# Performance work log

Hardware: AMD Instinct MI355X
Metric: run time of the kernel (lower is better)

The kernel has to match this reference:

```python
import jax, jax.numpy as jnp
import numpy as np

QSIGN = jnp.array([1.0, -1.0, -1.0, -1.0], dtype=jnp.float32)
IDENT = jnp.array([1.0, 0.0, 0.0, 0.0], dtype=jnp.float32)


def quat_multiply(a, b):
    aw, ax, ay, az = a[..., 0], a[..., 1], a[..., 2], a[..., 3]
    bw, bx, by, bz = b[..., 0], b[..., 1], b[..., 2], b[..., 3]
    return jnp.stack([
        aw * bw - ax * bx - ay * by - az * bz,
        aw * bx + ax * bw + ay * bz - az * by,
        aw * by - ax * bz + ay * bw + az * bx,
        aw * bz + ax * by - ay * bx + az * bw], axis=-1)


def quat_to_rot(q):
    w, x, y, z = q[..., 0], q[..., 1], q[..., 2], q[..., 3]
    r = jnp.stack([
        w * w + x * x - y * y - z * z, 2 * (x * y - w * z), 2 * (x * z + w * y),
        2 * (x * y + w * z), w * w - x * x + y * y - z * z, 2 * (y * z - w * x),
        2 * (x * z - w * y), 2 * (y * z + w * x), w * w - x * x - y * y + z * z], axis=-1)
    return r.reshape(q.shape[:-1] + (3, 3))


def quat_rotate(q, v):
    return jnp.einsum('...ij,...j->...i', quat_to_rot(q), v)


def mlp(z, W1, b1, W2, b2):
    return jax.nn.relu(z @ W1 + b1) @ W2 + b2


def setup_inputs() -> dict:
    key = jax.random.key(0)
    ks = jax.random.split(key, 24)
    B, N, H, E, M, O, T = 2, 512, 64, 32, 64, 64, 64
    x = jax.random.normal(ks[0], (B, N, 3), dtype=jnp.float32)
    q = jax.random.normal(ks[1], (B, N, 4), dtype=jnp.float32)
    q = q / jnp.linalg.norm(q, axis=-1, keepdims=True)  # unit quats
    h = jax.random.normal(ks[2], (B, N, H), dtype=jnp.float32)
    e = jax.random.normal(ks[3], (B, N, N, E), dtype=jnp.float32)
    node_mask = jnp.ones((B, N), dtype=bool)

    def lin(k, fi, fo):
        return jax.random.normal(k, (fi, fo), dtype=jnp.float32) / np.sqrt(fi)

    msg_in = 2 * H + E + 9  # 169
    inp = dict(x=x, quats=q, h=h, e=e, node_mask=node_mask,
               Wm1=lin(ks[4], msg_in, T), bm1=jnp.zeros((T,)),
               Wm2=lin(ks[5], T, M), bm2=jnp.zeros((M,)),
               Wf1=lin(ks[6], H + M, T), bf1=jnp.zeros((T,)),
               Wf2=lin(ks[7], T, O), bf2=jnp.zeros((O,)),
               Wt1=lin(ks[8], M, T), bt1=jnp.zeros((T,)),
               Wt2=lin(ks[9], T, 3), bt2=jnp.zeros((3,)),
               Wq1=lin(ks[10], M, T), bq1=jnp.zeros((T,)),
               Wq2=lin(ks[11], T, 4), bq2=jnp.zeros((4,)))
    return inp


def reference(x, quats, h, e, node_mask,
              Wm1, bm1, Wm2, bm2, Wf1, bf1, Wf2, bf2,
              Wt1, bt1, Wt2, bt2, Wq1, bq1, Wq2, bq2):
    B, N, H = h.shape
    eye = jnp.eye(N, dtype=bool)[None]
    msg_mask = node_mask[:, :, None] & node_mask[:, None, :] & ~eye  # [B,N,N]
    n_nodes = node_mask.sum(axis=-1).astype(x.dtype)  # [B]

    # inverse frame of node j: rot = conj(q_j)/|q_j|^2, applied as R_j^-1 (x_i - t_j)
    q_inv = (quats * QSIGN) / jnp.sum(quats * quats, axis=-1, keepdims=True)

    diff = x[:, :, None, :] - x[:, None, :, :]            # [B,N,N,3], x_i - x_j
    d2 = jnp.sum(diff * diff, axis=-1)                    # [B,N,N]
    qdot = jnp.abs(jnp.einsum('bik,bjk->bij', quats, quats))
    local_x = quat_rotate(q_inv[:, None, :, :], diff)     # R_j^-1 (x_i - x_j)
    local_q = quat_multiply(q_inv[:, None, :, :], quats[:, :, None, :])  # q_j^-1 * q_i

    hi = jnp.broadcast_to(h[:, :, None, :], (B, N, N, H))
    hj = jnp.broadcast_to(h[:, None, :, :], (B, N, N, H))
    feat = jnp.concatenate([hi, hj, e, local_x, local_q,
                            d2[..., None], qdot[..., None]], axis=-1)

    m = mlp(feat, Wm1, bm1, Wm2, bm2) * msg_mask[..., None]  # [B,N,N,M]
    msum = m.sum(axis=-2)                                    # [B,N,M]

    o = mlp(jnp.concatenate([h, msum], axis=-1), Wf1, bf1, Wf2, bf2)

    dx = mlp(m, Wt1, bt1, Wt2, bt2) * msg_mask[..., None]    # [B,N,N,3]

    dq = mlp(msum, Wq1, bq1, Wq2, bq2)                       # [B,N,4]
    dq = jnp.where(node_mask[..., None], dq, IDENT)
    dq = dq / jnp.maximum(jnp.linalg.norm(dq, axis=-1, keepdims=True), 1e-12)

    upd_q = quat_multiply(quats, dq)
    upd_q = jnp.where(node_mask[..., None], upd_q, IDENT)
    upd_q = upd_q / jnp.linalg.norm(upd_q, axis=-1, keepdims=True)  # normalize_quats=True

    # rotate dx[i,j] by updated frame of node j, aggregate over j
    rot_dx = quat_rotate(upd_q[:, None, :, :], dx).sum(axis=-2)     # [B,N,3]
    upd_x = x + rot_dx / (n_nodes[:, None, None] - 1.0)
    return upd_q, upd_x, o
```

## Files before the change

### kernel.cpp

```cpp
#include <hip/hip_runtime.h>
#include <math.h>
#include <stdint.h>

#define B_ 2
#define N_ 512

#define WS_QINV  0
#define WS_APRE  4096
#define WS_BPRET 69632
#define WS_UPDQ  135168
#define WS_MPART 139264
#define WS_DXBUF 270336

typedef short short8v __attribute__((ext_vector_type(8)));
typedef float f32x4 __attribute__((ext_vector_type(4)));

union FragU { int4 i; short8v s; };
union PackU { uint32_t w[4]; short8v s; };

static __device__ inline uint32_t pk2(float lo, float hi) {
    uint32_t r;
    asm volatile("v_cvt_pk_bf16_f32 %0, %1, %2" : "=v"(r) : "v"(lo), "v"(hi));
    return r;
}
static __device__ inline short f2bs(float f) {
    uint32_t u = __float_as_uint(f);
    u = (u + 0x7FFFu + ((u >> 16) & 1u)) >> 16;
    return (short)u;
}

__global__ __launch_bounds__(256) void k_node_pre(
    const float* __restrict__ quats,
    const float* __restrict__ h,
    const float* __restrict__ Wm1,
    const float* __restrict__ bm1,
    float* __restrict__ qinv,
    float* __restrict__ Apre,
    float* __restrict__ BpreT)
{
    __shared__ float sW[128 * 64];
    __shared__ float sh[4][64];

    const int tid = threadIdx.x;
    for (int idx = tid; idx < 128 * 64 / 4; idx += 256)
        ((float4*)sW)[idx] = ((const float4*)Wm1)[idx];

    const int wv = tid >> 6;
    const int c = tid & 63;
    const int node = blockIdx.x * 4 + wv;

    const float hv = h[node * 64 + c];
    sh[wv][c] = hv;
    __syncthreads();

    float a = bm1[c];
    float bv = 0.f;
#pragma unroll 8
    for (int k = 0; k < 64; ++k) {
        const float hk = sh[wv][k];
        a  = fmaf(hk, sW[k * 64 + c], a);
        bv = fmaf(hk, sW[(64 + k) * 64 + c], bv);
    }
    Apre[node * 64 + c] = a;
    BpreT[c * (B_ * N_) + node] = bv;

    if (c < 4) {
        const float qw = quats[node * 4 + 0];
        const float qx = quats[node * 4 + 1];
        const float qy = quats[node * 4 + 2];
        const float qz = quats[node * 4 + 3];
        const float d = qw * qw + qx * qx + qy * qy + qz * qz;
        const float sign = (c == 0) ? 1.f : -1.f;
        qinv[node * 4 + c] = quats[node * 4 + c] * sign / d;
    }
}

__global__ __launch_bounds__(256, 2) void k_edge(
    const float* __restrict__ x, const float* __restrict__ quats,
    const float* __restrict__ e,
    const float* __restrict__ Wm1, const float* __restrict__ Wm2,
    const float* __restrict__ bm2,
    const float* __restrict__ Wt1, const float* __restrict__ bt1,
    const float* __restrict__ Wt2, const float* __restrict__ bt2,
    const float* __restrict__ qinv, const float* __restrict__ Apre,
    const float* __restrict__ BpreT,
    float* __restrict__ mpart, float* __restrict__ dxbuf)
{
    __shared__ short W1s[64 * 72];
    __shared__ short W2s[64 * 72];
    __shared__ short W3s[64 * 72];
    __shared__ short W4s[16 * 72];
    __shared__ short featS[4][16 * 72];

    const int tid = threadIdx.x;

    for (int idx = tid; idx < 64 * 72; idx += 256) {
        const int ch = idx / 72, p = idx % 72;
        float v1 = 0.f, v2 = 0.f, v3 = 0.f;
        if (p < 64) {
            if (p < 32) v1 = Wm1[(128 + p) * 64 + ch];
            else if (p < 41) v1 = Wm1[(160 + p - 32) * 64 + ch];
            const int s = p >> 5, ee = p & 7, gg = (p >> 3) & 3;
            const int k1 = 32 * s + 16 * (ee >> 2) + 4 * gg + (ee & 3);
            v2 = Wm2[k1 * 64 + ch];
            v3 = Wt1[k1 * 64 + ch];
        }
        W1s[idx] = f2bs(v1); W2s[idx] = f2bs(v2); W3s[idx] = f2bs(v3);
    }
    for (int idx = tid; idx < 16 * 72; idx += 256) {
        const int d = idx / 72, p = idx % 72;
        float v = 0.f;
        if (p < 64 && d < 3) {
            const int s = p >> 5, ee = p & 7, gg = (p >> 3) & 3;
            const int k1 = 32 * s + 16 * (ee >> 2) + 4 * gg + (ee & 3);
            v = Wt2[k1 * 3 + d];
        }
        W4s[idx] = f2bs(v);
    }
    for (int idx = tid; idx < 4 * 16 * 72; idx += 256) (&featS[0][0])[idx] = 0;
    __syncthreads();

    const int w = tid >> 6;
    const int l = tid & 63;
    const int g = l >> 4;
    const int c = l & 15;

    const int ig = blockIdx.x >> 1;
    const int half = blockIdx.x & 1;
    const int ni = ig * 4 + w;
    const int b = ni >> 9;
    const int i = ni & 511;
    const int j0w = half * 256;

    short* fS = &featS[w][0];

    const float xi0 = x[ni * 3 + 0], xi1 = x[ni * 3 + 1], xi2 = x[ni * 3 + 2];
    const float qi0 = quats[ni * 4 + 0], qi1 = quats[ni * 4 + 1];
    const float qi2 = quats[ni * 4 + 2], qi3 = quats[ni * 4 + 3];

    float apre[16], bm2r[16], bt1r[16], bt2r[4];
#pragma unroll
    for (int q = 0; q < 16; ++q) {
        const int row = 16 * (q >> 2) + 4 * g + (q & 3);
        apre[q] = Apre[ni * 64 + row];
        bm2r[q] = bm2[row];
        bt1r[q] = bt1[row];
    }
#pragma unroll
    for (int q = 0; q < 4; ++q) {
        const int d = 4 * g + q;
        bt2r[q] = (d < 3) ? bt2[d] : 0.f;
    }

    float msum[16];
#pragma unroll
    for (int q = 0; q < 16; ++q) msum[q] = 0.f;

    for (int t = 0; t < 16; ++t) {
        const int j0m = j0w + t * 16;

        {
            const int je = l >> 2, kq = l & 3;
            const float* ep = e + (((size_t)(b * N_ + i)) * N_ + j0m + je) * 32 + kq * 8;
            const float4 v0 = *(const float4*)ep;
            const float4 v1 = *(const float4*)(ep + 4);
            int4 wv;
            wv.x = (int)pk2(v0.x, v0.y); wv.y = (int)pk2(v0.z, v0.w);
            wv.z = (int)pk2(v1.x, v1.y); wv.w = (int)pk2(v1.z, v1.w);
            *(int4*)&fS[je * 72 + kq * 8] = wv;
        }

        float bini[16];
#pragma unroll
        for (int q = 0; q < 16; ++q) {
            const int row = 16 * (q >> 2) + 4 * g + (q & 3);
            bini[q] = BpreT[row * (B_ * N_) + b * N_ + j0m + c];
        }

        {
            const int nj = b * N_ + j0m + c;
            const float xj0 = x[nj * 3 + 0], xj1 = x[nj * 3 + 1], xj2 = x[nj * 3 + 2];
            const float qj0 = quats[nj * 4 + 0], qj1 = quats[nj * 4 + 1];
            const float qj2 = quats[nj * 4 + 2], qj3 = quats[nj * 4 + 3];
            const float qw = qinv[nj * 4 + 0], qx = qinv[nj * 4 + 1];
            const float qy = qinv[nj * 4 + 2], qz = qinv[nj * 4 + 3];
            const float d0 = xi0 - xj0, d1 = xi1 - xj1, d2v = xi2 - xj2;
            const float dd = d0 * d0 + d1 * d1 + d2v * d2v;
            const float qd = fabsf(qi0 * qj0 + qi1 * qj1 + qi2 * qj2 + qi3 * qj3);
            const float ww = qw * qw, xx = qx * qx, yy = qy * qy, zz = qz * qz;
            const float xy = qx * qy, xz = qx * qz, yz = qy * qz;
            const float wx = qw * qx, wy = qw * qy, wz = qw * qz;
            const float lx0 = (ww + xx - yy - zz) * d0 + 2.f * (xy - wz) * d1 + 2.f * (xz + wy) * d2v;
            const float lx1 = 2.f * (xy + wz) * d0 + (ww - xx + yy - zz) * d1 + 2.f * (yz - wx) * d2v;
            const float lx2 = 2.f * (xz - wy) * d0 + 2.f * (yz + wx) * d1 + (ww - xx - yy + zz) * d2v;
            const float lq0 = qw * qi0 - qx * qi1 - qy * qi2 - qz * qi3;
            const float lq1 = qw * qi1 + qx * qi0 + qy * qi3 - qz * qi2;
            const float lq2 = qw * qi2 - qx * qi3 + qy * qi0 + qz * qi1;
            const float lq3 = qw * qi3 + qx * qi2 - qy * qi1 + qz * qi0;
            if (g == 0) {
                int4 wv;
                wv.x = (int)pk2(lx0, lx1); wv.y = (int)pk2(lx2, lq0);
                wv.z = (int)pk2(lq1, lq2); wv.w = (int)pk2(lq3, dd);
                *(int4*)&fS[c * 72 + 32] = wv;
                *(uint32_t*)&fS[c * 72 + 40] = pk2(qd, 0.f);
            }
        }
        asm volatile("s_waitcnt lgkmcnt(0)" ::: "memory");

        FragU y1[2];
#pragma unroll
        for (int s = 0; s < 2; ++s)
            y1[s].i = *(const int4*)&fS[c * 72 + s * 32 + g * 8];

        f32x4 acc1[4];
#pragma unroll
        for (int nt = 0; nt < 4; ++nt) {
            acc1[nt][0] = apre[nt * 4 + 0] + bini[nt * 4 + 0];
            acc1[nt][1] = apre[nt * 4 + 1] + bini[nt * 4 + 1];
            acc1[nt][2] = apre[nt * 4 + 2] + bini[nt * 4 + 2];
            acc1[nt][3] = apre[nt * 4 + 3] + bini[nt * 4 + 3];
        }
#pragma unroll
        for (int nt = 0; nt < 4; ++nt)
#pragma unroll
            for (int s = 0; s < 2; ++s) {
                FragU xw;
                xw.i = *(const int4*)&W1s[(16 * nt + c) * 72 + s * 32 + g * 8];
                acc1[nt] = __builtin_amdgcn_mfma_f32_16x16x32_bf16(
                    xw.s, y1[s].s, acc1[nt], 0, 0, 0);
            }

        PackU by1[2];
#pragma unroll
        for (int s = 0; s < 2; ++s) {
            const f32x4 a0 = acc1[2 * s], a1 = acc1[2 * s + 1];
            by1[s].w[0] = pk2(fmaxf(a0[0], 0.f), fmaxf(a0[1], 0.f));
            by1[s].w[1] = pk2(fmaxf(a0[2], 0.f), fmaxf(a0[3], 0.f));
            by1[s].w[2] = pk2(fmaxf(a1[0], 0.f), fmaxf(a1[1], 0.f));
            by1[s].w[3] = pk2(fmaxf(a1[2], 0.f), fmaxf(a1[3], 0.f));
        }

        f32x4 acc2[4];
#pragma unroll
        for (int nt = 0; nt < 4; ++nt) {
            acc2[nt][0] = bm2r[nt * 4 + 0]; acc2[nt][1] = bm2r[nt * 4 + 1];
            acc2[nt][2] = bm2r[nt * 4 + 2]; acc2[nt][3] = bm2r[nt * 4 + 3];
        }
#pragma unroll
        for (int nt = 0; nt < 4; ++nt)
#pragma unroll
            for (int s = 0; s < 2; ++s) {
                FragU xw;
                xw.i = *(const int4*)&W2s[(16 * nt + c) * 72 + s * 32 + g * 8];
                acc2[nt] = __builtin_amdgcn_mfma_f32_16x16x32_bf16(
                    xw.s, by1[s].s, acc2[nt], 0, 0, 0);
            }

        const float maskf = (j0m + c == i) ? 0.f : 1.f;
#pragma unroll
        for (int nt = 0; nt < 4; ++nt) {
            acc2[nt][0] *= maskf; acc2[nt][1] *= maskf;
            acc2[nt][2] *= maskf; acc2[nt][3] *= maskf;
            msum[nt * 4 + 0] += acc2[nt][0];
            msum[nt * 4 + 1] += acc2[nt][1];
            msum[nt * 4 + 2] += acc2[nt][2];
            msum[nt * 4 + 3] += acc2[nt][3];
        }

        PackU by2[2];
#pragma unroll
        for (int s = 0; s < 2; ++s) {
            const f32x4 a0 = acc2[2 * s], a1 = acc2[2 * s + 1];
            by2[s].w[0] = pk2(a0[0], a0[1]);
            by2[s].w[1] = pk2(a0[2], a0[3]);
            by2[s].w[2] = pk2(a1[0], a1[1]);
            by2[s].w[3] = pk2(a1[2], a1[3]);
        }

        f32x4 acc3[4];
#pragma unroll
        for (int nt = 0; nt < 4; ++nt) {
            acc3[nt][0] = bt1r[nt * 4 + 0]; acc3[nt][1] = bt1r[nt * 4 + 1];
            acc3[nt][2] = bt1r[nt * 4 + 2]; acc3[nt][3] = bt1r[nt * 4 + 3];
        }
#pragma unroll
        for (int nt = 0; nt < 4; ++nt)
#pragma unroll
            for (int s = 0; s < 2; ++s) {
                FragU xw;
                xw.i = *(const int4*)&W3s[(16 * nt + c) * 72 + s * 32 + g * 8];
                acc3[nt] = __builtin_amdgcn_mfma_f32_16x16x32_bf16(
                    xw.s, by2[s].s, acc3[nt], 0, 0, 0);
            }

        PackU by3[2];
#pragma unroll
        for (int s = 0; s < 2; ++s) {
            const f32x4 a0 = acc3[2 * s], a1 = acc3[2 * s + 1];
            by3[s].w[0] = pk2(fmaxf(a0[0], 0.f), fmaxf(a0[1], 0.f));
            by3[s].w[1] = pk2(fmaxf(a0[2], 0.f), fmaxf(a0[3], 0.f));
            by3[s].w[2] = pk2(fmaxf(a1[0], 0.f), fmaxf(a1[1], 0.f));
            by3[s].w[3] = pk2(fmaxf(a1[2], 0.f), fmaxf(a1[3], 0.f));
        }

        f32x4 acc4;
        acc4[0] = bt2r[0]; acc4[1] = bt2r[1]; acc4[2] = bt2r[2]; acc4[3] = bt2r[3];
#pragma unroll
        for (int s = 0; s < 2; ++s) {
            FragU xw;
            xw.i = *(const int4*)&W4s[c * 72 + s * 32 + g * 8];
            acc4 = __builtin_amdgcn_mfma_f32_16x16x32_bf16(
                xw.s, by3[s].s, acc4, 0, 0, 0);
        }
        if (g == 0) {
            float4 o4;
            o4.x = acc4[0] * maskf; o4.y = acc4[1] * maskf;
            o4.z = acc4[2] * maskf; o4.w = 0.f;
            ((float4*)dxbuf)[(size_t)ni * N_ + j0m + c] = o4;
        }
    }

#pragma unroll
    for (int q = 0; q < 16; ++q) {
        float v = msum[q];
        v += __shfl_xor(v, 1); v += __shfl_xor(v, 2);
        v += __shfl_xor(v, 4); v += __shfl_xor(v, 8);
        msum[q] = v;
    }
    if (c == 0) {
#pragma unroll
        for (int nt = 0; nt < 4; ++nt) {
            float4 mo;
            mo.x = msum[nt * 4 + 0]; mo.y = msum[nt * 4 + 1];
            mo.z = msum[nt * 4 + 2]; mo.w = msum[nt * 4 + 3];
            *(float4*)&mpart[((size_t)(half * (B_ * N_) + ni)) * 64 + 16 * nt + 4 * g] = mo;
        }
    }
}

__global__ __launch_bounds__(256) void k_node_post(
    const float* __restrict__ quats,
    const float* __restrict__ h,
    const float* __restrict__ mpart,
    const float* __restrict__ Wf1, const float* __restrict__ bf1,
    const float* __restrict__ Wf2, const float* __restrict__ bf2,
    const float* __restrict__ Wq1, const float* __restrict__ bq1,
    const float* __restrict__ Wq2, const float* __restrict__ bq2,
    float* __restrict__ updq,
    float* __restrict__ out_q, float* __restrict__ out_o)
{
    __shared__ float sWf1[128 * 64];
    __shared__ float sWf2[64 * 64];
    __shared__ float sWq1[64 * 64];
    __shared__ float sWq2[64 * 4];
    __shared__ float sh[4][64], sm[4][64], stf[4][64], stq[4][64];

    const int tid = threadIdx.x;
    for (int idx = tid; idx < 128 * 64 / 4; idx += 256)
        ((float4*)sWf1)[idx] = ((const float4*)Wf1)[idx];
    for (int idx = tid; idx < 64 * 64 / 4; idx += 256) {
        ((float4*)sWf2)[idx] = ((const float4*)Wf2)[idx];
        ((float4*)sWq1)[idx] = ((const float4*)Wq1)[idx];
    }
    if (tid < 64) sWq2[tid * 4 + 0] = Wq2[tid * 4 + 0],
                  sWq2[tid * 4 + 1] = Wq2[tid * 4 + 1],
                  sWq2[tid * 4 + 2] = Wq2[tid * 4 + 2],
                  sWq2[tid * 4 + 3] = Wq2[tid * 4 + 3];

    const int wv = tid >> 6;
    const int c = tid & 63;
    const int node = blockIdx.x * 4 + wv;

    const float ms = mpart[(size_t)node * 64 + c] +
                     mpart[((size_t)(B_ * N_) + node) * 64 + c];
    sm[wv][c] = ms;
    sh[wv][c] = h[node * 64 + c];
    __syncthreads();

    float accf = bf1[c];
    float accq = bq1[c];
#pragma unroll 8
    for (int k = 0; k < 64; ++k) {
        const float hk = sh[wv][k];
        const float mk = sm[wv][k];
        accf = fmaf(hk, sWf1[k * 64 + c], accf);
        accf = fmaf(mk, sWf1[(64 + k) * 64 + c], accf);
        accq = fmaf(mk, sWq1[k * 64 + c], accq);
    }
    stf[wv][c] = fmaxf(accf, 0.f);
    stq[wv][c] = fmaxf(accq, 0.f);
    __syncthreads();

    float o = bf2[c];
#pragma unroll 8
    for (int k = 0; k < 64; ++k) o = fmaf(stf[wv][k], sWf2[k * 64 + c], o);
    out_o[(size_t)node * 64 + c] = o;

    {
        const int d = c & 3, kb = c >> 2;
        float p = 0.f;
#pragma unroll
        for (int m = 0; m < 4; ++m) {
            const int kk = kb + 16 * m;
            p = fmaf(stq[wv][kk], sWq2[kk * 4 + d], p);
        }
        p += __shfl_xor(p, 4);  p += __shfl_xor(p, 8);
        p += __shfl_xor(p, 16); p += __shfl_xor(p, 32);
        const float p0 = __shfl(p, 0), p1 = __shfl(p, 1);
        const float p2 = __shfl(p, 2), p3 = __shfl(p, 3);
        if (c == 0) {
            float dq0 = p0 + bq2[0], dq1 = p1 + bq2[1];
            float dq2 = p2 + bq2[2], dq3 = p3 + bq2[3];
            const float nrm = sqrtf(dq0 * dq0 + dq1 * dq1 + dq2 * dq2 + dq3 * dq3);
            const float inv = 1.f / fmaxf(nrm, 1e-12f);
            const float b0 = dq0 * inv, b1 = dq1 * inv, b2 = dq2 * inv, b3 = dq3 * inv;
            const float aw = quats[node * 4 + 0], ax = quats[node * 4 + 1];
            const float ay = quats[node * 4 + 2], az = quats[node * 4 + 3];
            float u0 = aw * b0 - ax * b1 - ay * b2 - az * b3;
            float u1 = aw * b1 + ax * b0 + ay * b3 - az * b2;
            float u2 = aw * b2 - ax * b3 + ay * b0 + az * b1;
            float u3 = aw * b3 + ax * b2 - ay * b1 + az * b0;
            const float n2 = sqrtf(u0 * u0 + u1 * u1 + u2 * u2 + u3 * u3);
            u0 /= n2; u1 /= n2; u2 /= n2; u3 /= n2;
            out_q[node * 4 + 0] = u0; out_q[node * 4 + 1] = u1;
            out_q[node * 4 + 2] = u2; out_q[node * 4 + 3] = u3;
            updq[node * 4 + 0] = u0; updq[node * 4 + 1] = u1;
            updq[node * 4 + 2] = u2; updq[node * 4 + 3] = u3;
        }
    }
}

__global__ void k_aggregate(const float* __restrict__ x,
                            const float* __restrict__ updq,
                            const float* __restrict__ dxbuf,
                            float* __restrict__ out_x)
{
    const int node = blockIdx.x;
    const int b = node >> 9;
    const int tid = threadIdx.x;

    float s0 = 0.f, s1 = 0.f, s2 = 0.f;
    for (int j = tid; j < N_; j += 256) {
        const float4 d4 = ((const float4*)dxbuf)[(size_t)node * N_ + j];
        const float4 q4 = ((const float4*)updq)[b * N_ + j];
        const float w = q4.x, X = q4.y, Y = q4.z, Z = q4.w;
        const float ww = w * w, xx = X * X, yy = Y * Y, zz = Z * Z;
        const float xy = X * Y, xz = X * Z, yz = Y * Z;
        const float wx = w * X, wy = w * Y, wz = w * Z;
        s0 += (ww + xx - yy - zz) * d4.x + 2.f * (xy - wz) * d4.y + 2.f * (xz + wy) * d4.z;
        s1 += 2.f * (xy + wz) * d4.x + (ww - xx + yy - zz) * d4.y + 2.f * (yz - wx) * d4.z;
        s2 += 2.f * (xz - wy) * d4.x + 2.f * (yz + wx) * d4.y + (ww - xx - yy + zz) * d4.z;
    }
#pragma unroll
    for (int off = 1; off <= 32; off <<= 1) {
        s0 += __shfl_xor(s0, off);
        s1 += __shfl_xor(s1, off);
        s2 += __shfl_xor(s2, off);
    }
    __shared__ float red[4][3];
    const int wave = tid >> 6, lane = tid & 63;
    if (lane == 0) { red[wave][0] = s0; red[wave][1] = s1; red[wave][2] = s2; }
    __syncthreads();
    if (tid == 0) {
        const float t0 = red[0][0] + red[1][0] + red[2][0] + red[3][0];
        const float t1 = red[0][1] + red[1][1] + red[2][1] + red[3][1];
        const float t2 = red[0][2] + red[1][2] + red[2][2] + red[3][2];
        const float inv = 1.f / (float)(N_ - 1);
        out_x[node * 3 + 0] = x[node * 3 + 0] + t0 * inv;
        out_x[node * 3 + 1] = x[node * 3 + 1] + t1 * inv;
        out_x[node * 3 + 2] = x[node * 3 + 2] + t2 * inv;
    }
}

extern "C" void kernel_launch(void* const* d_in, const int* in_sizes, int n_in,
                              void* d_out, int out_size, void* d_ws, size_t ws_size,
                              hipStream_t stream) {
    const float* x     = (const float*)d_in[0];
    const float* quats = (const float*)d_in[1];
    const float* h     = (const float*)d_in[2];
    const float* e     = (const float*)d_in[3];
    const float* Wm1 = (const float*)d_in[5];
    const float* bm1 = (const float*)d_in[6];
    const float* Wm2 = (const float*)d_in[7];
    const float* bm2 = (const float*)d_in[8];
    const float* Wf1 = (const float*)d_in[9];
    const float* bf1 = (const float*)d_in[10];
    const float* Wf2 = (const float*)d_in[11];
    const float* bf2 = (const float*)d_in[12];
    const float* Wt1 = (const float*)d_in[13];
    const float* bt1 = (const float*)d_in[14];
    const float* Wt2 = (const float*)d_in[15];
    const float* bt2 = (const float*)d_in[16];
    const float* Wq1 = (const float*)d_in[17];
    const float* bq1 = (const float*)d_in[18];
    const float* Wq2 = (const float*)d_in[19];
    const float* bq2 = (const float*)d_in[20];

    float* out = (float*)d_out;
    float* out_q = out;
    float* out_x = out + 4096;
    float* out_o = out + 7168;

    float* ws    = (float*)d_ws;
    float* qinv  = ws + WS_QINV;
    float* Apre  = ws + WS_APRE;
    float* BpreT = ws + WS_BPRET;
    float* updq  = ws + WS_UPDQ;
    float* mpart = ws + WS_MPART;
    float* dxbuf = ws + WS_DXBUF;

    k_node_pre<<<dim3(B_ * N_ / 4), dim3(256), 0, stream>>>(
        quats, h, Wm1, bm1, qinv, Apre, BpreT);

    k_edge<<<dim3(512), dim3(256), 0, stream>>>(
        x, quats, e, Wm1, Wm2, bm2, Wt1, bt1, Wt2, bt2,
        qinv, Apre, BpreT, mpart, dxbuf);

    k_node_post<<<dim3(B_ * N_ / 4), dim3(256), 0, stream>>>(
        quats, h, mpart, Wf1, bf1, Wf2, bf2, Wq1, bq1, Wq2, bq2,
        updq, out_q, out_o);

    k_aggregate<<<dim3(B_ * N_), dim3(256), 0, stream>>>(
        x, updq, dxbuf, out_x);
}
```

Measured before the change: 186.8 us.

## Load edge features directly into MFMA fragments and repack node data for coalescing

The edge kernel no longer stages edge features and geometry through a per-wave LDS tile. Each lane now loads its own e slice and builds the bf16 MFMA operand in registers, removing LDS writes, waits and the tile zeroing. Node position and quaternion are packed into one 8-float record, and the Bpre term is stored in a fragment-ordered layout so each lane reads it as contiguous float4s; the quaternion inverse is computed inline with a fast reciprocal. The j range is split into quarters (1024 blocks, launch bound raised to 3 blocks per CU), and the post kernel sums four partial message sums. The cost is more partial-sum traffic, slightly lower precision in the inverse, and more register pressure under the higher occupancy target.

```diff
diff --git a/kernel.cpp b/kernel.cpp
--- a/kernel.cpp
+++ b/kernel.cpp
@@ -5,12 +5,11 @@
 #define B_ 2
 #define N_ 512
 
-#define WS_QINV  0
-#define WS_APRE  4096
-#define WS_BPRET 69632
-#define WS_UPDQ  135168
+#define WS_NGEO  0
+#define WS_APRE  8192
+#define WS_BPREF 73728
 #define WS_MPART 139264
-#define WS_DXBUF 270336
+#define WS_DXBUF 401408
 
 typedef short short8v __attribute__((ext_vector_type(8)));
 typedef float f32x4 __attribute__((ext_vector_type(4)));
@@ -30,13 +29,14 @@
 }
 
 __global__ __launch_bounds__(256) void k_node_pre(
+    const float* __restrict__ x,
     const float* __restrict__ quats,
     const float* __restrict__ h,
     const float* __restrict__ Wm1,
     const float* __restrict__ bm1,
-    float* __restrict__ qinv,
+    float* __restrict__ ngeo,
     float* __restrict__ Apre,
-    float* __restrict__ BpreT)
+    float* __restrict__ BpreF)
 {
     __shared__ float sW[128 * 64];
     __shared__ float sh[4][64];
@@ -49,8 +49,7 @@
     const int c = tid & 63;
     const int node = blockIdx.x * 4 + wv;
 
-    const float hv = h[node * 64 + c];
-    sh[wv][c] = hv;
+    sh[wv][c] = h[node * 64 + c];
     __syncthreads();
 
     float a = bm1[c];
@@ -62,35 +61,36 @@
         bv = fmaf(hk, sW[(64 + k) * 64 + c], bv);
     }
     Apre[node * 64 + c] = a;
-    BpreT[c * (B_ * N_) + node] = bv;
-
-    if (c < 4) {
-        const float qw = quats[node * 4 + 0];
-        const float qx = quats[node * 4 + 1];
-        const float qy = quats[node * 4 + 2];
-        const float qz = quats[node * 4 + 3];
-        const float d = qw * qw + qx * qx + qy * qy + qz * qz;
-        const float sign = (c == 0) ? 1.f : -1.f;
-        qinv[node * 4 + c] = quats[node * 4 + c] * sign / d;
-    }
-}
-
-__global__ __launch_bounds__(256, 2) void k_edge(
-    const float* __restrict__ x, const float* __restrict__ quats,
+    const int aa = c >> 4, gg = (c >> 2) & 3, bb = c & 3;
+    BpreF[(node >> 4) * 1024 + ((node & 15) + 16 * gg) * 16 + 4 * aa + bb] = bv;
+
+    if (c == 0) {
+        ngeo[node * 8 + 0] = x[node * 3 + 0];
+        ngeo[node * 8 + 1] = x[node * 3 + 1];
+        ngeo[node * 8 + 2] = x[node * 3 + 2];
+        ngeo[node * 8 + 3] = 0.f;
+        ngeo[node * 8 + 4] = quats[node * 4 + 0];
+        ngeo[node * 8 + 5] = quats[node * 4 + 1];
+        ngeo[node * 8 + 6] = quats[node * 4 + 2];
+        ngeo[node * 8 + 7] = quats[node * 4 + 3];
+    }
+}
+
+__global__ __launch_bounds__(256, 3) void k_edge(
     const float* __restrict__ e,
+    const float* __restrict__ ngeo,
+    const float* __restrict__ Apre,
+    const float* __restrict__ BpreF,
     const float* __restrict__ Wm1, const float* __restrict__ Wm2,
     const float* __restrict__ bm2,
     const float* __restrict__ Wt1, const float* __restrict__ bt1,
     const float* __restrict__ Wt2, const float* __restrict__ bt2,
-    const float* __restrict__ qinv, const float* __restrict__ Apre,
-    const float* __restrict__ BpreT,
     float* __restrict__ mpart, float* __restrict__ dxbuf)
 {
     __shared__ short W1s[64 * 72];
     __shared__ short W2s[64 * 72];
     __shared__ short W3s[64 * 72];
     __shared__ short W4s[16 * 72];
-    __shared__ short featS[4][16 * 72];
 
     const int tid = threadIdx.x;
 
@@ -117,7 +117,6 @@
         }
         W4s[idx] = f2bs(v);
     }
-    for (int idx = tid; idx < 4 * 16 * 72; idx += 256) (&featS[0][0])[idx] = 0;
     __syncthreads();
 
     const int w = tid >> 6;
@@ -125,18 +124,17 @@
     const int g = l >> 4;
     const int c = l & 15;
 
-    const int ig = blockIdx.x >> 1;
-    const int half = blockIdx.x & 1;
+    const int ig = blockIdx.x >> 2;
+    const int quarter = blockIdx.x & 3;
     const int ni = ig * 4 + w;
     const int b = ni >> 9;
     const int i = ni & 511;
-    const int j0w = half * 256;
-
-    short* fS = &featS[w][0];
-
-    const float xi0 = x[ni * 3 + 0], xi1 = x[ni * 3 + 1], xi2 = x[ni * 3 + 2];
-    const float qi0 = quats[ni * 4 + 0], qi1 = quats[ni * 4 + 1];
-    const float qi2 = quats[ni * 4 + 2], qi3 = quats[ni * 4 + 3];
+    const int j0w = quarter * 128;
+
+    const float4 gi0 = ((const float4*)ngeo)[ni * 2 + 0];
+    const float4 gi1 = ((const float4*)ngeo)[ni * 2 + 1];
+    const float xi0 = gi0.x, xi1 = gi0.y, xi2 = gi0.z;
+    const float qi0 = gi1.x, qi1 = gi1.y, qi2 = gi1.z, qi3 = gi1.w;
 
     float apre[16], bm2r[16], bt1r[16], bt2r[4];
 #pragma unroll
@@ -156,79 +154,70 @@
 #pragma unroll
     for (int q = 0; q < 16; ++q) msum[q] = 0.f;
 
-    for (int t = 0; t < 16; ++t) {
+#pragma unroll 2
+    for (int t = 0; t < 8; ++t) {
         const int j0m = j0w + t * 16;
-
-        {
-            const int je = l >> 2, kq = l & 3;
-            const float* ep = e + (((size_t)(b * N_ + i)) * N_ + j0m + je) * 32 + kq * 8;
-            const float4 v0 = *(const float4*)ep;
-            const float4 v1 = *(const float4*)(ep + 4);
-            int4 wv;
-            wv.x = (int)pk2(v0.x, v0.y); wv.y = (int)pk2(v0.z, v0.w);
-            wv.z = (int)pk2(v1.x, v1.y); wv.w = (int)pk2(v1.z, v1.w);
-            *(int4*)&fS[je * 72 + kq * 8] = wv;
-        }
-
-        float bini[16];
-#pragma unroll
-        for (int q = 0; q < 16; ++q) {
-            const int row = 16 * (q >> 2) + 4 * g + (q & 3);
-            bini[q] = BpreT[row * (B_ * N_) + b * N_ + j0m + c];
-        }
-
-        {
-            const int nj = b * N_ + j0m + c;
-            const float xj0 = x[nj * 3 + 0], xj1 = x[nj * 3 + 1], xj2 = x[nj * 3 + 2];
-            const float qj0 = quats[nj * 4 + 0], qj1 = quats[nj * 4 + 1];
-            const float qj2 = quats[nj * 4 + 2], qj3 = quats[nj * 4 + 3];
-            const float qw = qinv[nj * 4 + 0], qx = qinv[nj * 4 + 1];
-            const float qy = qinv[nj * 4 + 2], qz = qinv[nj * 4 + 3];
-            const float d0 = xi0 - xj0, d1 = xi1 - xj1, d2v = xi2 - xj2;
-            const float dd = d0 * d0 + d1 * d1 + d2v * d2v;
-            const float qd = fabsf(qi0 * qj0 + qi1 * qj1 + qi2 * qj2 + qi3 * qj3);
-            const float ww = qw * qw, xx = qx * qx, yy = qy * qy, zz = qz * qz;
-            const float xy = qx * qy, xz = qx * qz, yz = qy * qz;
-            const float wx = qw * qx, wy = qw * qy, wz = qw * qz;
-            const float lx0 = (ww + xx - yy - zz) * d0 + 2.f * (xy - wz) * d1 + 2.f * (xz + wy) * d2v;
-            const float lx1 = 2.f * (xy + wz) * d0 + (ww - xx + yy - zz) * d1 + 2.f * (yz - wx) * d2v;
-            const float lx2 = 2.f * (xz - wy) * d0 + 2.f * (yz + wx) * d1 + (ww - xx - yy + zz) * d2v;
-            const float lq0 = qw * qi0 - qx * qi1 - qy * qi2 - qz * qi3;
-            const float lq1 = qw * qi1 + qx * qi0 + qy * qi3 - qz * qi2;
-            const float lq2 = qw * qi2 - qx * qi3 + qy * qi0 + qz * qi1;
-            const float lq3 = qw * qi3 + qx * qi2 - qy * qi1 + qz * qi0;
-            if (g == 0) {
-                int4 wv;
-                wv.x = (int)pk2(lx0, lx1); wv.y = (int)pk2(lx2, lq0);
-                wv.z = (int)pk2(lq1, lq2); wv.w = (int)pk2(lq3, dd);
-                *(int4*)&fS[c * 72 + 32] = wv;
-                *(uint32_t*)&fS[c * 72 + 40] = pk2(qd, 0.f);
-            }
-        }
-        asm volatile("s_waitcnt lgkmcnt(0)" ::: "memory");
-
-        FragU y1[2];
-#pragma unroll
-        for (int s = 0; s < 2; ++s)
-            y1[s].i = *(const int4*)&fS[c * 72 + s * 32 + g * 8];
+        const int nj = b * N_ + j0m + c;
+
+        const float* ep = e + ((size_t)(b * N_ + i) * N_ + j0m + c) * 32 + g * 8;
+        const float4 e0 = *(const float4*)ep;
+        const float4 e1 = *(const float4*)(ep + 4);
+        const float4 n0 = ((const float4*)ngeo)[nj * 2 + 0];
+        const float4 n1 = ((const float4*)ngeo)[nj * 2 + 1];
+        const float* bp = BpreF + (size_t)(nj >> 4) * 1024 + l * 16;
+        const float4 bi0 = ((const float4*)bp)[0];
+        const float4 bi1 = ((const float4*)bp)[1];
+        const float4 bi2 = ((const float4*)bp)[2];
+        const float4 bi3 = ((const float4*)bp)[3];
+
+        const float xj0 = n0.x, xj1 = n0.y, xj2 = n0.z;
+        const float qj0 = n1.x, qj1 = n1.y, qj2 = n1.z, qj3 = n1.w;
+        const float dsum = qj0 * qj0 + qj1 * qj1 + qj2 * qj2 + qj3 * qj3;
+        const float inv = __builtin_amdgcn_rcpf(dsum);
+        const float qw = qj0 * inv, qx = -qj1 * inv;
+        const float qy = -qj2 * inv, qz = -qj3 * inv;
+        const float d0 = xi0 - xj0, d1 = xi1 - xj1, d2v = xi2 - xj2;
+        const float dd = d0 * d0 + d1 * d1 + d2v * d2v;
+        const float qd = fabsf(qi0 * qj0 + qi1 * qj1 + qi2 * qj2 + qi3 * qj3);
+        const float ww = qw * qw, xx = qx * qx, yy = qy * qy, zz = qz * qz;
+        const float xy = qx * qy, xz = qx * qz, yz = qy * qz;
+        const float wx = qw * qx, wy = qw * qy, wz = qw * qz;
+        const float lx0 = (ww + xx - yy - zz) * d0 + 2.f * (xy - wz) * d1 + 2.f * (xz + wy) * d2v;
+        const float lx1 = 2.f * (xy + wz) * d0 + (ww - xx + yy - zz) * d1 + 2.f * (yz - wx) * d2v;
+        const float lx2 = 2.f * (xz - wy) * d0 + 2.f * (yz + wx) * d1 + (ww - xx - yy + zz) * d2v;
+        const float lq0 = qw * qi0 - qx * qi1 - qy * qi2 - qz * qi3;
+        const float lq1 = qw * qi1 + qx * qi0 + qy * qi3 - qz * qi2;
+        const float lq2 = qw * qi2 - qx * qi3 + qy * qi0 + qz * qi1;
+        const float lq3 = qw * qi3 + qx * qi2 - qy * qi1 + qz * qi0;
+
+        PackU y0, yg;
+        y0.w[0] = pk2(e0.x, e0.y); y0.w[1] = pk2(e0.z, e0.w);
+        y0.w[2] = pk2(e1.x, e1.y); y0.w[3] = pk2(e1.z, e1.w);
+        const uint32_t w0 = pk2(lx0, lx1), w1 = pk2(lx2, lq0);
+        const uint32_t w2 = pk2(lq1, lq2), w3 = pk2(lq3, dd);
+        const uint32_t wq = pk2(qd, 0.f);
+        yg.w[0] = (g == 0) ? w0 : ((g == 1) ? wq : 0u);
+        yg.w[1] = (g == 0) ? w1 : 0u;
+        yg.w[2] = (g == 0) ? w2 : 0u;
+        yg.w[3] = (g == 0) ? w3 : 0u;
 
         f32x4 acc1[4];
+        acc1[0][0] = apre[0] + bi0.x;  acc1[0][1] = apre[1] + bi0.y;
+        acc1[0][2] = apre[2] + bi0.z;  acc1[0][3] = apre[3] + bi0.w;
+        acc1[1][0] = apre[4] + bi1.x;  acc1[1][1] = apre[5] + bi1.y;
+        acc1[1][2] = apre[6] + bi1.z;  acc1[1][3] = apre[7] + bi1.w;
+        acc1[2][0] = apre[8] + bi2.x;  acc1[2][1] = apre[9] + bi2.y;
+        acc1[2][2] = apre[10] + bi2.z; acc1[2][3] = apre[11] + bi2.w;
+        acc1[3][0] = apre[12] + bi3.x; acc1[3][1] = apre[13] + bi3.y;
+        acc1[3][2] = apre[14] + bi3.z; acc1[3][3] = apre[15] + bi3.w;
 #pragma unroll
         for (int nt = 0; nt < 4; ++nt) {
-            acc1[nt][0] = apre[nt * 4 + 0] + bini[nt * 4 + 0];
-            acc1[nt][1] = apre[nt * 4 + 1] + bini[nt * 4 + 1];
-            acc1[nt][2] = apre[nt * 4 + 2] + bini[nt * 4 + 2];
-            acc1[nt][3] = apre[nt * 4 + 3] + bini[nt * 4 + 3];
-        }
-#pragma unroll
-        for (int nt = 0; nt < 4; ++nt)
-#pragma unroll
-            for (int s = 0; s < 2; ++s) {
-                FragU xw;
-                xw.i = *(const int4*)&W1s[(16 * nt + c) * 72 + s * 32 + g * 8];
-                acc1[nt] = __builtin_amdgcn_mfma_f32_16x16x32_bf16(
-                    xw.s, y1[s].s, acc1[nt], 0, 0, 0);
-            }
+            FragU xw0, xw1;
+            xw0.i = *(const int4*)&W1s[(16 * nt + c) * 72 + g * 8];
+            xw1.i = *(const int4*)&W1s[(16 * nt + c) * 72 + 32 + g * 8];
+            acc1[nt] = __builtin_amdgcn_mfma_f32_16x16x32_bf16(xw0.s, y0.s, acc1[nt], 0, 0, 0);
+            acc1[nt] = __builtin_amdgcn_mfma_f32_16x16x32_bf16(xw1.s, yg.s, acc1[nt], 0, 0, 0);
+        }
 
         PackU by1[2];
 #pragma unroll
@@ -333,7 +322,7 @@
             float4 mo;
             mo.x = msum[nt * 4 + 0]; mo.y = msum[nt * 4 + 1];
             mo.z = msum[nt * 4 + 2]; mo.w = msum[nt * 4 + 3];
-            *(float4*)&mpart[((size_t)(half * (B_ * N_) + ni)) * 64 + 16 * nt + 4 * g] = mo;
+            *(float4*)&mpart[((size_t)(quarter * (B_ * N_) + ni)) * 64 + 16 * nt + 4 * g] = mo;
         }
     }
 }
@@ -346,7 +335,6 @@
     const float* __restrict__ Wf2, const float* __restrict__ bf2,
     const float* __restrict__ Wq1, const float* __restrict__ bq1,
     const float* __restrict__ Wq2, const float* __restrict__ bq2,
-    float* __restrict__ updq,
     float* __restrict__ out_q, float* __restrict__ out_o)
 {
     __shared__ float sWf1[128 * 64];
@@ -362,17 +350,21 @@
         ((float4*)sWf2)[idx] = ((const float4*)Wf2)[idx];
         ((float4*)sWq1)[idx] = ((const float4*)Wq1)[idx];
     }
-    if (tid < 64) sWq2[tid * 4 + 0] = Wq2[tid * 4 + 0],
-                  sWq2[tid * 4 + 1] = Wq2[tid * 4 + 1],
-                  sWq2[tid * 4 + 2] = Wq2[tid * 4 + 2],
-                  sWq2[tid * 4 + 3] = Wq2[tid * 4 + 3];
+    if (tid < 64) {
+        sWq2[tid * 4 + 0] = Wq2[tid * 4 + 0];
+        sWq2[tid * 4 + 1] = Wq2[tid * 4 + 1];
+        sWq2[tid * 4 + 2] = Wq2[tid * 4 + 2];
+        sWq2[tid * 4 + 3] = Wq2[tid * 4 + 3];
+    }
 
     const int wv = tid >> 6;
     const int c = tid & 63;
     const int node = blockIdx.x * 4 + wv;
 
     const float ms = mpart[(size_t)node * 64 + c] +
-                     mpart[((size_t)(B_ * N_) + node) * 64 + c];
+                     mpart[((size_t)(B_ * N_) + node) * 64 + c] +
+                     mpart[((size_t)(2 * B_ * N_) + node) * 64 + c] +
+                     mpart[((size_t)(3 * B_ * N_) + node) * 64 + c];
     sm[wv][c] = ms;
     sh[wv][c] = h[node * 64 + c];
     __syncthreads();
@@ -424,14 +416,12 @@
             u0 /= n2; u1 /= n2; u2 /= n2; u3 /= n2;
             out_q[node * 4 + 0] = u0; out_q[node * 4 + 1] = u1;
             out_q[node * 4 + 2] = u2; out_q[node * 4 + 3] = u3;
-            updq[node * 4 + 0] = u0; updq[node * 4 + 1] = u1;
-            updq[node * 4 + 2] = u2; updq[node * 4 + 3] = u3;
         }
     }
 }
 
 __global__ void k_aggregate(const float* __restrict__ x,
-                            const float* __restrict__ updq,
+                            const float* __restrict__ out_q,
                             const float* __restrict__ dxbuf,
                             float* __restrict__ out_x)
 {
@@ -442,7 +432,7 @@
     float s0 = 0.f, s1 = 0.f, s2 = 0.f;
     for (int j = tid; j < N_; j += 256) {
         const float4 d4 = ((const float4*)dxbuf)[(size_t)node * N_ + j];
-        const float4 q4 = ((const float4*)updq)[b * N_ + j];
+        const float4 q4 = ((const float4*)out_q)[b * N_ + j];
         const float w = q4.x, X = q4.y, Y = q4.z, Z = q4.w;
         const float ww = w * w, xx = X * X, yy = Y * Y, zz = Z * Z;
         const float xy = X * Y, xz = X * Z, yz = Y * Z;
@@ -502,24 +492,23 @@
     float* out_o = out + 7168;
 
     float* ws    = (float*)d_ws;
-    float* qinv  = ws + WS_QINV;
+    float* ngeo  = ws + WS_NGEO;
     float* Apre  = ws + WS_APRE;
-    float* BpreT = ws + WS_BPRET;
-    float* updq  = ws + WS_UPDQ;
+    float* BpreF = ws + WS_BPREF;
     float* mpart = ws + WS_MPART;
     float* dxbuf = ws + WS_DXBUF;
 
     k_node_pre<<<dim3(B_ * N_ / 4), dim3(256), 0, stream>>>(
-        quats, h, Wm1, bm1, qinv, Apre, BpreT);
-
-    k_edge<<<dim3(512), dim3(256), 0, stream>>>(
-        x, quats, e, Wm1, Wm2, bm2, Wt1, bt1, Wt2, bt2,
-        qinv, Apre, BpreT, mpart, dxbuf);
+        x, quats, h, Wm1, bm1, ngeo, Apre, BpreF);
+
+    k_edge<<<dim3(1024), dim3(256), 0, stream>>>(
+        e, ngeo, Apre, BpreF, Wm1, Wm2, bm2, Wt1, bt1, Wt2, bt2,
+        mpart, dxbuf);
 
     k_node_post<<<dim3(B_ * N_ / 4), dim3(256), 0, stream>>>(
         quats, h, mpart, Wf1, bf1, Wf2, bf2, Wq1, bq1, Wq2, bq2,
-        updq, out_q, out_o);
+        out_q, out_o);
 
     k_aggregate<<<dim3(B_ * N_), dim3(256), 0, stream>>>(
-        x, updq, dxbuf, out_x);
-}
+        x, out_q, dxbuf, out_x);
+}
```

Result: slower. 211.5 us (+13.2%).
